# Performance work log

Measured on AMD Instinct MI355X. Metric: run time of the kernel, lower is better.

## Reference

```python
import jax, jax.numpy as jnp
import numpy as np

B, LQ, LK = 4, 2048, 2048
DQ, DK, DO = 1024, 1024, 1024


def setup_inputs() -> dict:
    key = jax.random.key(0)
    ks = jax.random.split(key, 9)
    s = 0.02
    return {
        "query_input": jax.random.normal(ks[0], (B, LQ, DQ), jnp.float32),
        "key_input": jax.random.normal(ks[1], (B, LK, DK), jnp.float32),
        "value_input": jax.random.normal(ks[2], (B, LK, DK), jnp.float32),
        "Wq": jax.random.normal(ks[3], (DQ, DO), jnp.float32) * s,
        "bq": jax.random.normal(ks[4], (DO,), jnp.float32) * s,
        "Wk": jax.random.normal(ks[5], (DK, DO), jnp.float32) * s,
        "bk": jax.random.normal(ks[6], (DO,), jnp.float32) * s,
        "Wv": jax.random.normal(ks[7], (DK, DO), jnp.float32) * s,
        "bv": jax.random.normal(ks[8], (DO,), jnp.float32) * s,
    }


def reference(query_input, key_input, value_input, Wq, bq, Wk, bk, Wv, bv):
    scale = jnp.asarray(DO, query_input.dtype) ** 0.5
    q = query_input @ Wq + bq              # [B, Lq, D]
    k = key_input @ Wk + bk                # [B, Lk, D]
    v = value_input @ Wv + bv              # [B, Lk, D]
    attn = jnp.einsum("bqd,bkd->bqk", q, k) / scale
    attn = jax.nn.softmax(attn, axis=-1)
    return jnp.einsum("bqk,bkd->bqd", attn, v)
```

## Files before the change

kernel.cpp:

```cpp
#include <hip/hip_runtime.h>

typedef _Float16 f16x8 __attribute__((ext_vector_type(8)));
typedef _Float16 f16x4 __attribute__((ext_vector_type(4)));
typedef float f32x4 __attribute__((ext_vector_type(4)));

__device__ __forceinline__ void lds_load16(const _Float16* g, _Float16* l) {
    __builtin_amdgcn_global_load_lds(
        (const __attribute__((address_space(1))) void*)g,
        (__attribute__((address_space(3))) void*)l,
        16, 0, 0);
}

template <int MODE>
__global__ __launch_bounds__(256, 2)
void gemm_core(const _Float16* A, const _Float16* B, void* Cv, const float* bias,
               const _Float16* Ax1, const _Float16* Bx1, void* Cx1, const float* bx1,
               const _Float16* Ax2, const _Float16* Bx2, void* Cx2, const float* bx2,
               float* rowsum)
{
    const int z = blockIdx.z;
    size_t cbase = 0;
    int lda, ldb, K, m0, n0;
    if (MODE == 0) {
        if (z == 1) { A = Ax1; B = Bx1; Cv = Cx1; bias = bx1; }
        else if (z == 2) { A = Ax2; B = Bx2; Cv = Cx2; bias = bx2; }
        lda = 1024; ldb = 1024; K = 1024;
        m0 = (z == 2 ? blockIdx.x : blockIdx.y) * 128;
        n0 = (z == 2 ? blockIdx.y : blockIdx.x) * 128;
    } else if (MODE == 3) {
        A += (size_t)z * 2048 * 1024;
        B += (size_t)z * 2048 * 1024;
        cbase = (size_t)z * 2048 * 2048;
        rowsum += z * 2048;
        lda = 1024; ldb = 1024; K = 1024;
        m0 = blockIdx.y * 128; n0 = blockIdx.x * 128;
    } else {
        A += (size_t)z * 2048 * 2048;
        B += (size_t)z * 2048;
        cbase = (size_t)z * 2048 * 1024;
        rowsum += z * 2048;
        lda = 2048; ldb = 8192; K = 2048;
        m0 = blockIdx.y * 128; n0 = blockIdx.x * 128;
    }

    __shared__ __align__(16) _Float16 As[128 * 32];
    __shared__ __align__(16) _Float16 Bs[128 * 32];

    const int t    = threadIdx.x;
    const int w    = t >> 6;
    const int lane = t & 63;
    const int ln   = lane & 15;
    const int kq   = lane >> 4;
    const int wm   = (w & 1) * 64;
    const int wn   = (w >> 1) * 64;

    const int arow = t >> 2;
    const int kcf  = (t & 3) * 8;
    const _Float16* gA0 = A + (size_t)(m0 + arow) * lda + kcf;
    const _Float16* gA1 = A + (size_t)(m0 + 64 + arow) * lda + kcf;
    const _Float16* gB0 = B + (size_t)(n0 + arow) * ldb + kcf;
    const _Float16* gB1 = B + (size_t)(n0 + 64 + arow) * ldb + kcf;
    _Float16* lA0 = As + w * 512;
    _Float16* lA1 = As + 2048 + w * 512;
    _Float16* lB0 = Bs + w * 512;
    _Float16* lB1 = Bs + 2048 + w * 512;

    f32x4 acc[4][4] = {};

    for (int k0 = 0; k0 < K; k0 += 32) {
        __syncthreads();
        lds_load16(gA0 + k0, lA0);
        lds_load16(gA1 + k0, lA1);
        lds_load16(gB0 + k0, lB0);
        lds_load16(gB1 + k0, lB1);
        __syncthreads();

        f16x8 af[4], bf[4];
#pragma unroll
        for (int i = 0; i < 4; ++i)
            af[i] = *(const f16x8*)(As + (wm + i * 16 + ln) * 32 + kq * 8);
#pragma unroll
        for (int i = 0; i < 4; ++i)
            bf[i] = *(const f16x8*)(Bs + (wn + i * 16 + ln) * 32 + kq * 8);
#pragma unroll
        for (int i = 0; i < 4; ++i)
#pragma unroll
            for (int j = 0; j < 4; ++j)
                acc[i][j] = __builtin_amdgcn_mfma_f32_16x16x32_f16(af[i], bf[j], acc[i][j], 0, 0, 0);
    }

    const int ldc = (MODE == 0) ? (z == 2 ? 8192 : 1024)
                  : (MODE == 3) ? 2048 : 1024;
    float*    Cf = (float*)Cv;
    _Float16* Ch = (_Float16*)Cv;
#pragma unroll
    for (int i = 0; i < 4; ++i) {
        const int rbase = m0 + wm + i * 16 + kq * 4;

        if (MODE == 0) {
#pragma unroll
            for (int j = 0; j < 4; ++j) {
                const int gcol = n0 + wn + j * 16 + ln;
#pragma unroll
                for (int r = 0; r < 4; ++r) {
                    float vv = acc[i][j][r] + (z == 2 ? bias[rbase + r] : bias[gcol]);
                    Ch[(size_t)(rbase + r) * ldc + gcol] = (_Float16)vv;
                }
            }
        } else if (MODE == 3) {
            float rs[4] = {0.f, 0.f, 0.f, 0.f};
#pragma unroll
            for (int j = 0; j < 4; ++j) {
                const int gcol = n0 + wn + j * 16 + ln;
#pragma unroll
                for (int r = 0; r < 4; ++r) {
                    float e = __expf(acc[i][j][r] * 0.03125f);
                    Ch[cbase + (size_t)(rbase + r) * ldc + gcol] = (_Float16)e;
                    rs[r] += e;
                }
            }
#pragma unroll
            for (int r = 0; r < 4; ++r) {
                float s = rs[r];
                s += __shfl_xor(s, 1);
                s += __shfl_xor(s, 2);
                s += __shfl_xor(s, 4);
                s += __shfl_xor(s, 8);
                if (ln == 0) atomicAdd(&rowsum[rbase + r], s);
            }
        } else {
            float inv[4];
#pragma unroll
            for (int r = 0; r < 4; ++r) inv[r] = 1.f / rowsum[rbase + r];
#pragma unroll
            for (int j = 0; j < 4; ++j) {
                const int gcol = n0 + wn + j * 16 + ln;
#pragma unroll
                for (int r = 0; r < 4; ++r)
                    Cf[cbase + (size_t)(rbase + r) * ldc + gcol] = acc[i][j][r] * inv[r];
            }
        }
    }
}

__global__ __launch_bounds__(256)
void cvt_f16(const float4* __restrict__ x0, _Float16* __restrict__ y0,
             const float4* __restrict__ x1, _Float16* __restrict__ y1,
             const float4* __restrict__ x2, _Float16* __restrict__ y2,
             float* __restrict__ rowsum)
{
    const size_t i = (size_t)blockIdx.x * 256 + threadIdx.x;
    const float4* x = blockIdx.y == 0 ? x0 : blockIdx.y == 1 ? x1 : x2;
    _Float16*    yy = blockIdx.y == 0 ? y0 : blockIdx.y == 1 ? y1 : y2;
    float4 f = x[i];
    f16x4 o = { (_Float16)f.x, (_Float16)f.y, (_Float16)f.z, (_Float16)f.w };
    *(f16x4*)(yy + i * 4) = o;
    if (blockIdx.y == 0 && blockIdx.x < 32)
        rowsum[blockIdx.x * 256 + threadIdx.x] = 0.f;
}

__global__ __launch_bounds__(256)
void transpose_w_1024(const float* __restrict__ W0, _Float16* __restrict__ T0,
                      const float* __restrict__ W1, _Float16* __restrict__ T1,
                      const float* __restrict__ W2, _Float16* __restrict__ T2)
{
    const float* W = blockIdx.z == 0 ? W0 : blockIdx.z == 1 ? W1 : W2;
    _Float16*   WT = blockIdx.z == 0 ? T0 : blockIdx.z == 1 ? T1 : T2;
    __shared__ float tile[32][33];
    const int bx = blockIdx.x * 32;
    const int by = blockIdx.y * 32;
    const int tx = threadIdx.x;
    const int ty = threadIdx.y;
#pragma unroll
    for (int i = ty; i < 32; i += 8)
        tile[i][tx] = W[(size_t)(by + i) * 1024 + bx + tx];
    __syncthreads();
#pragma unroll
    for (int i = ty; i < 32; i += 8)
        WT[(size_t)(bx + i) * 1024 + by + tx] = (_Float16)tile[tx][i];
}

extern "C" void kernel_launch(void* const* d_in, const int* in_sizes, int n_in,
                              void* d_out, int out_size, void* d_ws, size_t ws_size,
                              hipStream_t stream)
{
    const float* Xq = (const float*)d_in[0];
    const float* Xk = (const float*)d_in[1];
    const float* Xv = (const float*)d_in[2];
    const float* Wq = (const float*)d_in[3];
    const float* bq = (const float*)d_in[4];
    const float* Wk = (const float*)d_in[5];
    const float* bk = (const float*)d_in[6];
    const float* Wv = (const float*)d_in[7];
    const float* bv = (const float*)d_in[8];
    float* out = (float*)d_out;

    const size_t XN = (size_t)8192 * 1024;
    const size_t WN = (size_t)1024 * 1024;

    _Float16* ws  = (_Float16*)d_ws;
    _Float16* Xqh = ws;
    _Float16* Xkh = Xqh + XN;
    _Float16* Xvh = Xkh + XN;
    _Float16* WqT = Xvh + XN;
    _Float16* WkT = WqT + WN;
    _Float16* WvT = WkT + WN;
    _Float16* qh  = WvT + WN;
    _Float16* kh  = qh + XN;
    _Float16* vT  = kh + XN;
    _Float16* S   = vT + XN;
    float* rowsum = (float*)(S + (size_t)4 * 2048 * 2048);

    {
        dim3 g(8192, 3);
        cvt_f16<<<g, 256, 0, stream>>>((const float4*)Xq, Xqh,
                                       (const float4*)Xk, Xkh,
                                       (const float4*)Xv, Xvh, rowsum);
    }

    {
        dim3 tb(32, 8), tg(32, 32, 3);
        transpose_w_1024<<<tg, tb, 0, stream>>>(Wq, WqT, Wk, WkT, Wv, WvT);
    }

    {
        dim3 g(8, 64, 3);
        gemm_core<0><<<g, 256, 0, stream>>>(
            Xqh, WqT, qh, bq,
            Xkh, WkT, kh, bk,
            WvT, Xvh, vT, bv,
            nullptr);
    }

    {
        dim3 g(16, 16, 4);
        gemm_core<3><<<g, 256, 0, stream>>>(
            qh, kh, S, nullptr,
            nullptr, nullptr, nullptr, nullptr,
            nullptr, nullptr, nullptr, nullptr,
            rowsum);
    }

    {
        dim3 g(8, 16, 4);
        gemm_core<5><<<g, 256, 0, stream>>>(
            S, vT, out, nullptr,
            nullptr, nullptr, nullptr, nullptr,
            nullptr, nullptr, nullptr, nullptr,
            rowsum);
    }
}
```

Before: 342.3 us.

## Double-buffer LDS tiles, swizzle block-to-tile mapping, raise occupancy hint

The GEMM main loop now double-buffers the A/B LDS tiles. The next K-slice's global-to-LDS loads are issued before the current slice's MFMAs, so each iteration needs one barrier instead of two and load latency overlaps with compute. Block indices are remapped into grouped tile orders in all three GEMM modes, so concurrently running blocks share A/B rows and columns for better L2 reuse. The launch-bounds occupancy hint goes from 2 to 4 blocks per CU. That doubles LDS per block and tightens the register budget, which risks spills given the 64-float accumulator.

```diff
diff --git a/kernel.cpp b/kernel.cpp
--- a/kernel.cpp
+++ b/kernel.cpp
@@ -12,39 +12,46 @@
 }
 
 template <int MODE>
-__global__ __launch_bounds__(256, 2)
+__global__ __launch_bounds__(256, 4)
 void gemm_core(const _Float16* A, const _Float16* B, void* Cv, const float* bias,
                const _Float16* Ax1, const _Float16* Bx1, void* Cx1, const float* bx1,
                const _Float16* Ax2, const _Float16* Bx2, void* Cx2, const float* bx2,
                float* rowsum)
 {
     const int z = blockIdx.z;
+    const int bx = blockIdx.x, by = blockIdx.y;
     size_t cbase = 0;
     int lda, ldb, K, m0, n0;
     if (MODE == 0) {
+        const int tmy = bx * 8 + (by >> 3);
+        const int tnx = by & 7;
         if (z == 1) { A = Ax1; B = Bx1; Cv = Cx1; bias = bx1; }
         else if (z == 2) { A = Ax2; B = Bx2; Cv = Cx2; bias = bx2; }
         lda = 1024; ldb = 1024; K = 1024;
-        m0 = (z == 2 ? blockIdx.x : blockIdx.y) * 128;
-        n0 = (z == 2 ? blockIdx.y : blockIdx.x) * 128;
+        m0 = (z == 2 ? tnx : tmy) * 128;
+        n0 = (z == 2 ? tmy : tnx) * 128;
     } else if (MODE == 3) {
+        const int tm = (bx & 7) * 2 + (by >> 3);
+        const int tn = (bx >> 3) * 8 + (by & 7);
         A += (size_t)z * 2048 * 1024;
         B += (size_t)z * 2048 * 1024;
         cbase = (size_t)z * 2048 * 2048;
         rowsum += z * 2048;
         lda = 1024; ldb = 1024; K = 1024;
-        m0 = blockIdx.y * 128; n0 = blockIdx.x * 128;
+        m0 = tm * 128; n0 = tn * 128;
     } else {
+        const int tm = bx * 2 + (by >> 3);
+        const int tn = by & 7;
         A += (size_t)z * 2048 * 2048;
         B += (size_t)z * 2048;
         cbase = (size_t)z * 2048 * 1024;
         rowsum += z * 2048;
         lda = 2048; ldb = 8192; K = 2048;
-        m0 = blockIdx.y * 128; n0 = blockIdx.x * 128;
-    }
-
-    __shared__ __align__(16) _Float16 As[128 * 32];
-    __shared__ __align__(16) _Float16 Bs[128 * 32];
+        m0 = tm * 128; n0 = tn * 128;
+    }
+
+    __shared__ __align__(16) _Float16 As[2][128 * 32];
+    __shared__ __align__(16) _Float16 Bs[2][128 * 32];
 
     const int t    = threadIdx.x;
     const int w    = t >> 6;
@@ -60,33 +67,38 @@
     const _Float16* gA1 = A + (size_t)(m0 + 64 + arow) * lda + kcf;
     const _Float16* gB0 = B + (size_t)(n0 + arow) * ldb + kcf;
     const _Float16* gB1 = B + (size_t)(n0 + 64 + arow) * ldb + kcf;
-    _Float16* lA0 = As + w * 512;
-    _Float16* lA1 = As + 2048 + w * 512;
-    _Float16* lB0 = Bs + w * 512;
-    _Float16* lB1 = Bs + 2048 + w * 512;
+
+    auto stage = [&](int buf, int k0) {
+        lds_load16(gA0 + k0, As[buf] + w * 512);
+        lds_load16(gA1 + k0, As[buf] + 2048 + w * 512);
+        lds_load16(gB0 + k0, Bs[buf] + w * 512);
+        lds_load16(gB1 + k0, Bs[buf] + 2048 + w * 512);
+    };
 
     f32x4 acc[4][4] = {};
 
+    stage(0, 0);
+    int cur = 0;
+#pragma unroll 2
     for (int k0 = 0; k0 < K; k0 += 32) {
         __syncthreads();
-        lds_load16(gA0 + k0, lA0);
-        lds_load16(gA1 + k0, lA1);
-        lds_load16(gB0 + k0, lB0);
-        lds_load16(gB1 + k0, lB1);
-        __syncthreads();
-
+        if (k0 + 32 < K) stage(cur ^ 1, k0 + 32);
+
+        const _Float16* Ab = As[cur];
+        const _Float16* Bb = Bs[cur];
         f16x8 af[4], bf[4];
 #pragma unroll
         for (int i = 0; i < 4; ++i)
-            af[i] = *(const f16x8*)(As + (wm + i * 16 + ln) * 32 + kq * 8);
+            af[i] = *(const f16x8*)(Ab + (wm + i * 16 + ln) * 32 + kq * 8);
 #pragma unroll
         for (int i = 0; i < 4; ++i)
-            bf[i] = *(const f16x8*)(Bs + (wn + i * 16 + ln) * 32 + kq * 8);
+            bf[i] = *(const f16x8*)(Bb + (wn + i * 16 + ln) * 32 + kq * 8);
 #pragma unroll
         for (int i = 0; i < 4; ++i)
 #pragma unroll
             for (int j = 0; j < 4; ++j)
                 acc[i][j] = __builtin_amdgcn_mfma_f32_16x16x32_f16(af[i], bf[j], acc[i][j], 0, 0, 0);
+        cur ^= 1;
     }
 
     const int ldc = (MODE == 0) ? (z == 2 ? 8192 : 1024)
```

After: 333.0 us. 2.7% less time.
